# Kernel optimization log

Hardware: AMD Instinct MI355X
Metric: run time of the kernel (lower is better)

The kernel has to match this reference:

```python
import jax, jax.numpy as jnp
import numpy as np

EMBED_DIM = 1024
NUM_HEADS = 16
HEAD_DIM = EMBED_DIM // NUM_HEADS


def setup_inputs() -> dict:
    key = jax.random.key(0)
    ks = jax.random.split(key, 5)
    s = 0.02
    return {
        "x": jax.random.normal(ks[0], (2, 2048, EMBED_DIM), dtype=jnp.float32),
        "w_qkv": jax.random.normal(ks[1], (EMBED_DIM, 3 * EMBED_DIM), dtype=jnp.float32) * s,
        "b_qkv": jnp.zeros((3 * EMBED_DIM,), dtype=jnp.float32),
        "w_out": jax.random.normal(ks[2], (EMBED_DIM, EMBED_DIM), dtype=jnp.float32) * s,
        "b_out": jnp.zeros((EMBED_DIM,), dtype=jnp.float32),
    }


def reference(x, w_qkv, b_qkv, w_out, b_out):
    B, T, C = x.shape
    qkv = x @ w_qkv + b_qkv                       # [B,T,3C]
    q, k, v = jnp.split(qkv, 3, axis=-1)
    # [B,T,C] -> [B,H,T,Dh]
    def heads(t):
        return t.reshape(B, T, NUM_HEADS, HEAD_DIM).transpose(0, 2, 1, 3)
    q, k, v = heads(q), heads(k), heads(v)
    scale = 1.0 / np.sqrt(HEAD_DIM).astype(np.float32)
    scores = jnp.einsum("bhqd,bhkd->bhqk", q, k) * scale  # [B,H,T,T]
    causal = jnp.tril(jnp.ones((T, T), dtype=bool))
    scores = jnp.where(causal[None, None], scores, -jnp.inf)
    attn = jax.nn.softmax(scores, axis=-1)
    out = jnp.einsum("bhqk,bhkd->bhqd", attn, v)  # [B,H,T,Dh]
    out = out.transpose(0, 2, 1, 3).reshape(B, T, C)
    return out @ w_out + b_out
```

## Files before the change

kernel.cpp:

```cpp
#include <hip/hip_runtime.h>

typedef unsigned short u16;
typedef unsigned int u32;
typedef __attribute__((ext_vector_type(8))) short bf16x8;
typedef __attribute__((ext_vector_type(4))) float f32x4;

#define TOK   4096
#define EMB   1024
#define NQKV  3072
#define TSEQ  2048
#define NH    16

__device__ __forceinline__ u16 f2b(float f) {
  union { float f; unsigned u; } v; v.f = f;
  unsigned r = v.u + 0x7FFFu + ((v.u >> 16) & 1u);
  return (u16)(r >> 16);
}

__device__ __forceinline__ u32 pack_rn(float a, float b) {
  u32 ua = __float_as_uint(a) + 0x8000u;
  u32 ub = __float_as_uint(b) + 0x8000u;
  return __builtin_amdgcn_perm(ub, ua, 0x07060302u);
}


__global__ __launch_bounds__(256) void cvt_f32_bf16(const float* __restrict__ x,
                                                    u16* __restrict__ y, int n4) {
  int i = blockIdx.x * 256 + threadIdx.x;
  if (i < n4) {
    float4 v = ((const float4*)x)[i];
    union { u16 us[4]; uint2 u2; } o;
    o.us[0] = f2b(v.x); o.us[1] = f2b(v.y); o.us[2] = f2b(v.z); o.us[3] = f2b(v.w);
    ((uint2*)y)[i] = o.u2;
  }
}

__global__ __launch_bounds__(256) void transpose_f32_bf16(const float* __restrict__ src,
                                                          u16* __restrict__ dst,
                                                          int R, int C) {
  __shared__ u16 sm[64][65];
  int c0 = blockIdx.x * 64, r0 = blockIdx.y * 64;
  int tid = threadIdx.x;
#pragma unroll
  for (int i = 0; i < 16; i++) {
    int idx = tid + i * 256;
    int r = idx >> 6, c = idx & 63;
    sm[r][c] = f2b(src[(size_t)(r0 + r) * C + c0 + c]);
  }
  __syncthreads();
#pragma unroll
  for (int i = 0; i < 16; i++) {
    int idx = tid + i * 256;
    int cc = idx >> 6, rr = idx & 63;
    dst[(size_t)(c0 + cc) * R + r0 + rr] = sm[rr][cc];
  }
}

__global__ __launch_bounds__(256) void transpose_v(const u16* __restrict__ V,
                                                   u16* __restrict__ Vt) {
  __shared__ u16 sm[64][72];
  int t0 = blockIdx.x * 64, bh = blockIdx.y;
  size_t base = (size_t)bh * TSEQ * 64;
  int tid = threadIdx.x;
  int r = tid >> 2, c = (tid & 3) * 16;
  *(bf16x8*)&sm[r][c]     = *(const bf16x8*)&V[base + (size_t)(t0 + r) * 64 + c];
  *(bf16x8*)&sm[r][c + 8] = *(const bf16x8*)&V[base + (size_t)(t0 + r) * 64 + c + 8];
  __syncthreads();
  int d = tid >> 2, tc = (tid & 3) * 16;
  union { u16 us[16]; uint4 v4[2]; } o;
#pragma unroll
  for (int i = 0; i < 16; i++) o.us[i] = sm[tc + i][d];
  *(uint4*)&Vt[base + (size_t)d * TSEQ + t0 + tc]     = o.v4[0];
  *(uint4*)&Vt[base + (size_t)d * TSEQ + t0 + tc + 8] = o.v4[1];
}


template <int MODE, int TM>
__global__ __launch_bounds__(256) void gemm_bt(const u16* __restrict__ A,
                                               const u16* __restrict__ Bt,
                                               const float* __restrict__ bias,
                                               u16* __restrict__ qb, u16* __restrict__ kb,
                                               u16* __restrict__ vb, float* __restrict__ outp,
                                               int K, int N) {
  constexpr int LDA = 68;
  constexpr int CT = (TM == 128) ? 4 : 2;
  constexpr int AC = TM / 32;
  __shared__ u16 As[TM][LDA];
  __shared__ u16 Bs[128][LDA];
  int tid = threadIdx.x;
  int m0 = blockIdx.y * TM, n0 = blockIdx.x * 128;
  int lane = tid & 63, wid = tid >> 6;
  int wm = (TM == 128) ? (wid >> 1) * 64 : 0;
  int wn = (TM == 128) ? (wid & 1) * 64 : wid * 32;
  int l15 = lane & 15, quad = lane >> 4;
  int lrow = lane >> 3, lcol = (lane & 7) * 8;

  f32x4 acc[4][CT];
#pragma unroll
  for (int i = 0; i < 4; i++)
#pragma unroll
    for (int j = 0; j < CT; j++) acc[i][j] = (f32x4){0.f, 0.f, 0.f, 0.f};

  bf16x8 ar[AC], br[4];
#pragma unroll
  for (int i = 0; i < AC; i++)
    ar[i] = *(const bf16x8*)&A[(size_t)(m0 + (wid * AC + i) * 8 + lrow) * K + lcol];
#pragma unroll
  for (int i = 0; i < 4; i++)
    br[i] = *(const bf16x8*)&Bt[(size_t)(n0 + (wid * 4 + i) * 8 + lrow) * K + lcol];

  for (int k0 = 0; k0 < K; k0 += 64) {
#pragma unroll
    for (int i = 0; i < AC; i++)
      *(bf16x8*)&As[(wid * AC + i) * 8 + lrow][lcol] = ar[i];
#pragma unroll
    for (int i = 0; i < 4; i++)
      *(bf16x8*)&Bs[(wid * 4 + i) * 8 + lrow][lcol] = br[i];
    __syncthreads();

    if (k0 + 64 < K) {
      int kn = k0 + 64;
#pragma unroll
      for (int i = 0; i < AC; i++)
        ar[i] = *(const bf16x8*)&A[(size_t)(m0 + (wid * AC + i) * 8 + lrow) * K + kn + lcol];
#pragma unroll
      for (int i = 0; i < 4; i++)
        br[i] = *(const bf16x8*)&Bt[(size_t)(n0 + (wid * 4 + i) * 8 + lrow) * K + kn + lcol];
    }

#pragma unroll
    for (int ks = 0; ks < 2; ks++) {
      bf16x8 af[4], bfr[CT];
#pragma unroll
      for (int rt = 0; rt < 4; rt++)
        af[rt] = *(const bf16x8*)&As[wm + rt * 16 + l15][ks * 32 + quad * 8];
#pragma unroll
      for (int ct = 0; ct < CT; ct++)
        bfr[ct] = *(const bf16x8*)&Bs[wn + ct * 16 + l15][ks * 32 + quad * 8];
#pragma unroll
      for (int rt = 0; rt < 4; rt++)
#pragma unroll
        for (int ct = 0; ct < CT; ct++)
          acc[rt][ct] = __builtin_amdgcn_mfma_f32_16x16x32_bf16(bfr[ct], af[rt], acc[rt][ct], 0, 0, 0);
    }
    __syncthreads();
  }

#pragma unroll
  for (int rt = 0; rt < 4; rt++) {
#pragma unroll
    for (int ct = 0; ct < CT; ct++) {
      int m = m0 + wm + rt * 16 + l15;
      int nb = n0 + wn + ct * 16 + quad * 4;
      float4 b4 = *(const float4*)&bias[nb];
      float v0 = acc[rt][ct][0] + b4.x, v1 = acc[rt][ct][1] + b4.y;
      float v2 = acc[rt][ct][2] + b4.z, v3 = acc[rt][ct][3] + b4.w;
      if (MODE == 0) {
        int sel = nb >> 10;
        int c = nb & 1023;
        int h = c >> 6, d0 = c & 63;
        int b = m >> 11, t = m & 2047;
        u16* dst = (sel == 0) ? qb : (sel == 1) ? kb : vb;
        union { u32 u[2]; uint2 u2; } o;
        o.u[0] = pack_rn(v0, v1);
        o.u[1] = pack_rn(v2, v3);
        *(uint2*)&dst[((((size_t)b * NH + h) * TSEQ + t) << 6) + d0] = o.u2;
      } else {
        float4 o = {v0, v1, v2, v3};
        *(float4*)&outp[(size_t)m * N + nb] = o;
      }
    }
  }
}


__global__ __launch_bounds__(256) void attn_kernel(const u16* __restrict__ Qb,
                                                   const u16* __restrict__ Kb,
                                                   const u16* __restrict__ Vtb,
                                                   u16* __restrict__ O) {
  __shared__ u16 Ks[64][68];
  __shared__ u16 Vt[64][68];
  __shared__ u16 Ps[4][16][68];

  const float SCL = 0.18033688f;
  const float MOFF = 16.0f;

  int id = blockIdx.x;
  int bh = (id >> 5) & 31;
  int q5 = id & 31;
  int qt = ((id >> 8) & 1) ? (31 - q5) : q5;

  int tid = threadIdx.x, lane = tid & 63, w = tid >> 6;
  int l15 = lane & 15, quad = lane >> 4;
  const size_t hoff = (size_t)bh * TSEQ * 64;

  int qrow = qt * 64 + w * 16 + l15;
  bf16x8 qf[2];
  qf[0] = *(const bf16x8*)&Qb[hoff + (size_t)qrow * 64 + quad * 8];
  qf[1] = *(const bf16x8*)&Qb[hoff + (size_t)qrow * 64 + 32 + quad * 8];

  f32x4 acc[4];
#pragma unroll
  for (int i = 0; i < 4; i++) acc[i] = (f32x4){0.f, 0.f, 0.f, 0.f};
  float l_i = 0.f;

  int srow = tid >> 2, scol = (tid & 3) * 16;

  bf16x8 kr0, kr1, vr0, vr1;
  {
    size_t kg = hoff + (size_t)srow * 64;
    kr0 = *(const bf16x8*)&Kb[kg + scol];
    kr1 = *(const bf16x8*)&Kb[kg + scol + 8];
    size_t vg = hoff + (size_t)srow * TSEQ;
    vr0 = *(const bf16x8*)&Vtb[vg + scol];
    vr1 = *(const bf16x8*)&Vtb[vg + scol + 8];
  }

  for (int kt = 0; kt <= qt; kt++) {
    __syncthreads();
    *(bf16x8*)&Ks[srow][scol]     = kr0;
    *(bf16x8*)&Ks[srow][scol + 8] = kr1;
    *(bf16x8*)&Vt[srow][scol]     = vr0;
    *(bf16x8*)&Vt[srow][scol + 8] = vr1;
    __syncthreads();
    if (kt < qt) {
      size_t kg = hoff + (size_t)((kt + 1) * 64 + srow) * 64;
      kr0 = *(const bf16x8*)&Kb[kg + scol];
      kr1 = *(const bf16x8*)&Kb[kg + scol + 8];
      size_t vg = hoff + (size_t)srow * TSEQ + (kt + 1) * 64;
      vr0 = *(const bf16x8*)&Vtb[vg + scol];
      vr1 = *(const bf16x8*)&Vtb[vg + scol + 8];
    }

    f32x4 s[4];
#pragma unroll
    for (int ct = 0; ct < 4; ct++) s[ct] = (f32x4){0.f, 0.f, 0.f, 0.f};
#pragma unroll
    for (int ks = 0; ks < 2; ks++)
#pragma unroll
      for (int ct = 0; ct < 4; ct++) {
        bf16x8 kf = *(const bf16x8*)&Ks[ct * 16 + l15][ks * 32 + quad * 8];
        s[ct] = __builtin_amdgcn_mfma_f32_16x16x32_bf16(kf, qf[ks], s[ct], 0, 0, 0);
      }

    if (kt == qt) {
      int ql = w * 16 + l15;
#pragma unroll
      for (int ct = 0; ct < 4; ct++)
#pragma unroll
        for (int r = 0; r < 4; r++)
          if (ct * 16 + quad * 4 + r > ql) s[ct][r] = -1e30f;
    }

    float rs = 0.f;
#pragma unroll
    for (int ct = 0; ct < 4; ct++)
#pragma unroll
      for (int r = 0; r < 4; r++) {
        float p = exp2f(__builtin_fmaf(s[ct][r], SCL, -MOFF));
        s[ct][r] = p;
        rs += p;
      }
    l_i += rs;

#pragma unroll
    for (int ct = 0; ct < 4; ct++) {
      *(u32*)&Ps[w][l15][ct * 16 + quad * 4]     = pack_rn(s[ct][0], s[ct][1]);
      *(u32*)&Ps[w][l15][ct * 16 + quad * 4 + 2] = pack_rn(s[ct][2], s[ct][3]);
    }
    bf16x8 pf0 = *(const bf16x8*)&Ps[w][l15][quad * 8];
    bf16x8 pf1 = *(const bf16x8*)&Ps[w][l15][32 + quad * 8];
#pragma unroll
    for (int dt = 0; dt < 4; dt++) {
      bf16x8 vf0 = *(const bf16x8*)&Vt[dt * 16 + l15][quad * 8];
      bf16x8 vf1 = *(const bf16x8*)&Vt[dt * 16 + l15][32 + quad * 8];
      acc[dt] = __builtin_amdgcn_mfma_f32_16x16x32_bf16(vf0, pf0, acc[dt], 0, 0, 0);
      acc[dt] = __builtin_amdgcn_mfma_f32_16x16x32_bf16(vf1, pf1, acc[dt], 0, 0, 0);
    }
  }

  l_i += __shfl_xor(l_i, 16);
  l_i += __shfl_xor(l_i, 32);
  float inv = 1.0f / l_i;

  int b = bh >> 4, h = bh & 15;
  int qg = qt * 64 + w * 16 + l15;
  size_t rowbase = ((size_t)b * TSEQ + qg) * 1024 + h * 64;
#pragma unroll
  for (int dt = 0; dt < 4; dt++) {
    union { u32 u[2]; uint2 u2; } o;
    o.u[0] = pack_rn(acc[dt][0] * inv, acc[dt][1] * inv);
    o.u[1] = pack_rn(acc[dt][2] * inv, acc[dt][3] * inv);
    *(uint2*)&O[rowbase + dt * 16 + quad * 4] = o.u2;
  }
}


extern "C" void kernel_launch(void* const* d_in, const int* in_sizes, int n_in,
                              void* d_out, int out_size, void* d_ws, size_t ws_size,
                              hipStream_t stream) {
  (void)in_sizes; (void)n_in; (void)out_size; (void)ws_size;
  const float* x     = (const float*)d_in[0];
  const float* w_qkv = (const float*)d_in[1];
  const float* b_qkv = (const float*)d_in[2];
  const float* w_out = (const float*)d_in[3];
  const float* b_out = (const float*)d_in[4];
  float* out = (float*)d_out;

  char* p = (char*)d_ws;
  u16* x_bf  = (u16*)p; p += (size_t)TOK * EMB * 2;
  u16* wqkvT = (u16*)p; p += (size_t)NQKV * EMB * 2;
  u16* woutT = (u16*)p; p += (size_t)EMB * EMB * 2;
  u16* Qb    = (u16*)p; p += (size_t)32 * TSEQ * 64 * 2;
  u16* Kb    = (u16*)p; p += (size_t)32 * TSEQ * 64 * 2;
  u16* Vraw  = (u16*)p; p += (size_t)32 * TSEQ * 64 * 2;
  u16* attn_o = (u16*)p;
  u16* Vtb   = x_bf;

  cvt_f32_bf16<<<dim3(TOK * EMB / 1024), 256, 0, stream>>>(x, x_bf, TOK * EMB / 4);
  transpose_f32_bf16<<<dim3(NQKV / 64, EMB / 64), 256, 0, stream>>>(w_qkv, wqkvT, EMB, NQKV);
  transpose_f32_bf16<<<dim3(EMB / 64, EMB / 64), 256, 0, stream>>>(w_out, woutT, EMB, EMB);
  gemm_bt<0, 128><<<dim3(NQKV / 128, TOK / 128), 256, 0, stream>>>(x_bf, wqkvT, b_qkv,
                                                                   Qb, Kb, Vraw, nullptr, EMB, NQKV);
  transpose_v<<<dim3(TSEQ / 64, 32), 256, 0, stream>>>(Vraw, Vtb);
  attn_kernel<<<dim3(1024), 256, 0, stream>>>(Qb, Kb, Vtb, attn_o);
  gemm_bt<1, 64><<<dim3(EMB / 128, TOK / 64), 256, 0, stream>>>(attn_o, woutT, b_out,
                                                                nullptr, nullptr, nullptr, out, EMB, EMB);
}
```

Before: 195.3 us.

## Load K/V fragments directly from global in attention and fuse prep kernels

The attention kernel no longer stages K and V tiles through shared memory with block-wide barriers. Each wave now reads its MFMA operand fragments straight from global memory, relying on L1/L2 to serve the reuse across the four waves. The P stores to shared memory are widened to 64-bit writes. Separately, the input conversion and the two weight transposes are merged into one launch to cut launch overhead. The trade-off is fewer syncs and less LDS traffic against redundant, less coalesced global loads and no explicit prefetch of the next tile.

```diff
diff --git a/kernel.cpp b/kernel.cpp
--- a/kernel.cpp
+++ b/kernel.cpp
@@ -24,23 +24,31 @@
 }
 
 
-__global__ __launch_bounds__(256) void cvt_f32_bf16(const float* __restrict__ x,
-                                                    u16* __restrict__ y, int n4) {
-  int i = blockIdx.x * 256 + threadIdx.x;
-  if (i < n4) {
+__global__ __launch_bounds__(256) void prep_kernel(const float* __restrict__ x,
+                                                   u16* __restrict__ x_bf,
+                                                   const float* __restrict__ w_qkv,
+                                                   u16* __restrict__ wqkvT,
+                                                   const float* __restrict__ w_out,
+                                                   u16* __restrict__ woutT) {
+  __shared__ u16 sm[64][65];
+  int bid = blockIdx.x, tid = threadIdx.x;
+  if (bid < 4096) {
+    int i = bid * 256 + tid;
     float4 v = ((const float4*)x)[i];
     union { u16 us[4]; uint2 u2; } o;
     o.us[0] = f2b(v.x); o.us[1] = f2b(v.y); o.us[2] = f2b(v.z); o.us[3] = f2b(v.w);
-    ((uint2*)y)[i] = o.u2;
-  }
-}
-
-__global__ __launch_bounds__(256) void transpose_f32_bf16(const float* __restrict__ src,
-                                                          u16* __restrict__ dst,
-                                                          int R, int C) {
-  __shared__ u16 sm[64][65];
-  int c0 = blockIdx.x * 64, r0 = blockIdx.y * 64;
-  int tid = threadIdx.x;
+    ((uint2*)x_bf)[i] = o.u2;
+    return;
+  }
+  const float* src; u16* dst; int R, C, bx, by;
+  if (bid < 4096 + 768) {
+    int t = bid - 4096; bx = t % 48; by = t / 48;
+    src = w_qkv; dst = wqkvT; R = EMB; C = NQKV;
+  } else {
+    int t = bid - 4096 - 768; bx = t & 15; by = t >> 4;
+    src = w_out; dst = woutT; R = EMB; C = EMB;
+  }
+  int c0 = bx * 64, r0 = by * 64;
 #pragma unroll
   for (int i = 0; i < 16; i++) {
     int idx = tid + i * 256;
@@ -178,8 +186,6 @@
                                                    const u16* __restrict__ Kb,
                                                    const u16* __restrict__ Vtb,
                                                    u16* __restrict__ O) {
-  __shared__ u16 Ks[64][68];
-  __shared__ u16 Vt[64][68];
   __shared__ u16 Ps[4][16][68];
 
   const float SCL = 0.18033688f;
@@ -204,44 +210,19 @@
   for (int i = 0; i < 4; i++) acc[i] = (f32x4){0.f, 0.f, 0.f, 0.f};
   float l_i = 0.f;
 
-  int srow = tid >> 2, scol = (tid & 3) * 16;
-
-  bf16x8 kr0, kr1, vr0, vr1;
-  {
-    size_t kg = hoff + (size_t)srow * 64;
-    kr0 = *(const bf16x8*)&Kb[kg + scol];
-    kr1 = *(const bf16x8*)&Kb[kg + scol + 8];
-    size_t vg = hoff + (size_t)srow * TSEQ;
-    vr0 = *(const bf16x8*)&Vtb[vg + scol];
-    vr1 = *(const bf16x8*)&Vtb[vg + scol + 8];
-  }
+  const u16* kp = Kb + hoff + (size_t)l15 * 64 + quad * 8;
+  const u16* vp = Vtb + hoff + (size_t)l15 * TSEQ + quad * 8;
 
   for (int kt = 0; kt <= qt; kt++) {
-    __syncthreads();
-    *(bf16x8*)&Ks[srow][scol]     = kr0;
-    *(bf16x8*)&Ks[srow][scol + 8] = kr1;
-    *(bf16x8*)&Vt[srow][scol]     = vr0;
-    *(bf16x8*)&Vt[srow][scol + 8] = vr1;
-    __syncthreads();
-    if (kt < qt) {
-      size_t kg = hoff + (size_t)((kt + 1) * 64 + srow) * 64;
-      kr0 = *(const bf16x8*)&Kb[kg + scol];
-      kr1 = *(const bf16x8*)&Kb[kg + scol + 8];
-      size_t vg = hoff + (size_t)srow * TSEQ + (kt + 1) * 64;
-      vr0 = *(const bf16x8*)&Vtb[vg + scol];
-      vr1 = *(const bf16x8*)&Vtb[vg + scol + 8];
-    }
-
     f32x4 s[4];
 #pragma unroll
-    for (int ct = 0; ct < 4; ct++) s[ct] = (f32x4){0.f, 0.f, 0.f, 0.f};
-#pragma unroll
-    for (int ks = 0; ks < 2; ks++)
-#pragma unroll
-      for (int ct = 0; ct < 4; ct++) {
-        bf16x8 kf = *(const bf16x8*)&Ks[ct * 16 + l15][ks * 32 + quad * 8];
-        s[ct] = __builtin_amdgcn_mfma_f32_16x16x32_bf16(kf, qf[ks], s[ct], 0, 0, 0);
-      }
+    for (int ct = 0; ct < 4; ct++) {
+      bf16x8 kf0 = *(const bf16x8*)&kp[ct * 16 * 64];
+      bf16x8 kf1 = *(const bf16x8*)&kp[ct * 16 * 64 + 32];
+      f32x4 z = (f32x4){0.f, 0.f, 0.f, 0.f};
+      z = __builtin_amdgcn_mfma_f32_16x16x32_bf16(kf0, qf[0], z, 0, 0, 0);
+      s[ct] = __builtin_amdgcn_mfma_f32_16x16x32_bf16(kf1, qf[1], z, 0, 0, 0);
+    }
 
     if (kt == qt) {
       int ql = w * 16 + l15;
@@ -265,18 +246,23 @@
 
 #pragma unroll
     for (int ct = 0; ct < 4; ct++) {
-      *(u32*)&Ps[w][l15][ct * 16 + quad * 4]     = pack_rn(s[ct][0], s[ct][1]);
-      *(u32*)&Ps[w][l15][ct * 16 + quad * 4 + 2] = pack_rn(s[ct][2], s[ct][3]);
+      union { u32 u[2]; uint2 u2; } o;
+      o.u[0] = pack_rn(s[ct][0], s[ct][1]);
+      o.u[1] = pack_rn(s[ct][2], s[ct][3]);
+      *(uint2*)&Ps[w][l15][ct * 16 + quad * 4] = o.u2;
     }
     bf16x8 pf0 = *(const bf16x8*)&Ps[w][l15][quad * 8];
     bf16x8 pf1 = *(const bf16x8*)&Ps[w][l15][32 + quad * 8];
 #pragma unroll
     for (int dt = 0; dt < 4; dt++) {
-      bf16x8 vf0 = *(const bf16x8*)&Vt[dt * 16 + l15][quad * 8];
-      bf16x8 vf1 = *(const bf16x8*)&Vt[dt * 16 + l15][32 + quad * 8];
+      bf16x8 vf0 = *(const bf16x8*)&vp[(size_t)dt * 16 * TSEQ];
+      bf16x8 vf1 = *(const bf16x8*)&vp[(size_t)dt * 16 * TSEQ + 32];
       acc[dt] = __builtin_amdgcn_mfma_f32_16x16x32_bf16(vf0, pf0, acc[dt], 0, 0, 0);
       acc[dt] = __builtin_amdgcn_mfma_f32_16x16x32_bf16(vf1, pf1, acc[dt], 0, 0, 0);
     }
+
+    kp += 64 * 64;
+    vp += 64;
   }
 
   l_i += __shfl_xor(l_i, 16);
@@ -317,9 +303,7 @@
   u16* attn_o = (u16*)p;
   u16* Vtb   = x_bf;
 
-  cvt_f32_bf16<<<dim3(TOK * EMB / 1024), 256, 0, stream>>>(x, x_bf, TOK * EMB / 4);
-  transpose_f32_bf16<<<dim3(NQKV / 64, EMB / 64), 256, 0, stream>>>(w_qkv, wqkvT, EMB, NQKV);
-  transpose_f32_bf16<<<dim3(EMB / 64, EMB / 64), 256, 0, stream>>>(w_out, woutT, EMB, EMB);
+  prep_kernel<<<dim3(4096 + 768 + 256), 256, 0, stream>>>(x, x_bf, w_qkv, wqkvT, w_out, woutT);
   gemm_bt<0, 128><<<dim3(NQKV / 128, TOK / 128), 256, 0, stream>>>(x_bf, wqkvT, b_qkv,
                                                                    Qb, Kb, Vraw, nullptr, EMB, NQKV);
   transpose_v<<<dim3(TSEQ / 64, 32), 256, 0, stream>>>(Vraw, Vtb);
```

New measurement: 269.3 us. +37.9%, slower.

## Double query tile per attention block and merge prep kernels into one launch

Applied to the files above, without the earlier changes.

The attention kernel now handles 128 query rows per block, with each wave owning two 16-row query groups, so every K/V tile staged in shared memory serves twice as many queries. The grid is halved to 512 blocks and remapped so paired query tiles balance the causal work. The three input conversion and transpose kernels are merged into one launch to save launch overhead. The cost is more registers per wave and fewer blocks, which may reduce occupancy and latency hiding.

```diff
diff --git a/kernel.cpp b/kernel.cpp
--- a/kernel.cpp
+++ b/kernel.cpp
@@ -24,23 +24,31 @@
 }
 
 
-__global__ __launch_bounds__(256) void cvt_f32_bf16(const float* __restrict__ x,
-                                                    u16* __restrict__ y, int n4) {
-  int i = blockIdx.x * 256 + threadIdx.x;
-  if (i < n4) {
+__global__ __launch_bounds__(256) void prep_kernel(const float* __restrict__ x,
+                                                   u16* __restrict__ x_bf,
+                                                   const float* __restrict__ w_qkv,
+                                                   u16* __restrict__ wqkvT,
+                                                   const float* __restrict__ w_out,
+                                                   u16* __restrict__ woutT) {
+  __shared__ u16 sm[64][65];
+  int bid = blockIdx.x, tid = threadIdx.x;
+  if (bid < 4096) {
+    int i = bid * 256 + tid;
     float4 v = ((const float4*)x)[i];
     union { u16 us[4]; uint2 u2; } o;
     o.us[0] = f2b(v.x); o.us[1] = f2b(v.y); o.us[2] = f2b(v.z); o.us[3] = f2b(v.w);
-    ((uint2*)y)[i] = o.u2;
-  }
-}
-
-__global__ __launch_bounds__(256) void transpose_f32_bf16(const float* __restrict__ src,
-                                                          u16* __restrict__ dst,
-                                                          int R, int C) {
-  __shared__ u16 sm[64][65];
-  int c0 = blockIdx.x * 64, r0 = blockIdx.y * 64;
-  int tid = threadIdx.x;
+    ((uint2*)x_bf)[i] = o.u2;
+    return;
+  }
+  const float* src; u16* dst; int R, C, bx, by;
+  if (bid < 4096 + 768) {
+    int t = bid - 4096; bx = t % 48; by = t / 48;
+    src = w_qkv; dst = wqkvT; R = EMB; C = NQKV;
+  } else {
+    int t = bid - 4096 - 768; bx = t & 15; by = t >> 4;
+    src = w_out; dst = woutT; R = EMB; C = EMB;
+  }
+  int c0 = bx * 64, r0 = by * 64;
 #pragma unroll
   for (int i = 0; i < 16; i++) {
     int idx = tid + i * 256;
@@ -180,31 +188,40 @@
                                                    u16* __restrict__ O) {
   __shared__ u16 Ks[64][68];
   __shared__ u16 Vt[64][68];
-  __shared__ u16 Ps[4][16][68];
+  __shared__ u16 Ps[4][2][16][68];
 
   const float SCL = 0.18033688f;
   const float MOFF = 16.0f;
 
   int id = blockIdx.x;
-  int bh = (id >> 5) & 31;
-  int q5 = id & 31;
-  int qt = ((id >> 8) & 1) ? (31 - q5) : q5;
+  int bh = id & 31;
+  int qq = id >> 5;
+  int Qt = (qq < 8) ? qq : 23 - qq;
 
   int tid = threadIdx.x, lane = tid & 63, w = tid >> 6;
   int l15 = lane & 15, quad = lane >> 4;
   const size_t hoff = (size_t)bh * TSEQ * 64;
 
-  int qrow = qt * 64 + w * 16 + l15;
-  bf16x8 qf[2];
-  qf[0] = *(const bf16x8*)&Qb[hoff + (size_t)qrow * 64 + quad * 8];
-  qf[1] = *(const bf16x8*)&Qb[hoff + (size_t)qrow * 64 + 32 + quad * 8];
-
-  f32x4 acc[4];
-#pragma unroll
-  for (int i = 0; i < 4; i++) acc[i] = (f32x4){0.f, 0.f, 0.f, 0.f};
-  float l_i = 0.f;
+  int q0 = Qt * 128 + w * 32;
+  bf16x8 qfA0, qfA1, qfB0, qfB1;
+  {
+    const u16* qp = Qb + hoff + (size_t)(q0 + l15) * 64 + quad * 8;
+    qfA0 = *(const bf16x8*)qp;
+    qfA1 = *(const bf16x8*)(qp + 32);
+    qfB0 = *(const bf16x8*)(qp + 16 * 64);
+    qfB1 = *(const bf16x8*)(qp + 16 * 64 + 32);
+  }
+
+  f32x4 accA[4], accB[4];
+#pragma unroll
+  for (int i = 0; i < 4; i++) {
+    accA[i] = (f32x4){0.f, 0.f, 0.f, 0.f};
+    accB[i] = (f32x4){0.f, 0.f, 0.f, 0.f};
+  }
+  float lA = 0.f, lB = 0.f;
 
   int srow = tid >> 2, scol = (tid & 3) * 16;
+  const int KT = 2 * Qt + 2;
 
   bf16x8 kr0, kr1, vr0, vr1;
   {
@@ -216,14 +233,14 @@
     vr1 = *(const bf16x8*)&Vtb[vg + scol + 8];
   }
 
-  for (int kt = 0; kt <= qt; kt++) {
+  for (int kt = 0; kt < KT; kt++) {
     __syncthreads();
     *(bf16x8*)&Ks[srow][scol]     = kr0;
     *(bf16x8*)&Ks[srow][scol + 8] = kr1;
     *(bf16x8*)&Vt[srow][scol]     = vr0;
     *(bf16x8*)&Vt[srow][scol + 8] = vr1;
     __syncthreads();
-    if (kt < qt) {
+    if (kt + 1 < KT) {
       size_t kg = hoff + (size_t)((kt + 1) * 64 + srow) * 64;
       kr0 = *(const bf16x8*)&Kb[kg + scol];
       kr1 = *(const bf16x8*)&Kb[kg + scol + 8];
@@ -232,66 +249,91 @@
       vr1 = *(const bf16x8*)&Vtb[vg + scol + 8];
     }
 
-    f32x4 s[4];
-#pragma unroll
-    for (int ct = 0; ct < 4; ct++) s[ct] = (f32x4){0.f, 0.f, 0.f, 0.f};
-#pragma unroll
-    for (int ks = 0; ks < 2; ks++)
-#pragma unroll
-      for (int ct = 0; ct < 4; ct++) {
-        bf16x8 kf = *(const bf16x8*)&Ks[ct * 16 + l15][ks * 32 + quad * 8];
-        s[ct] = __builtin_amdgcn_mfma_f32_16x16x32_bf16(kf, qf[ks], s[ct], 0, 0, 0);
+    f32x4 sA[4], sB[4];
+#pragma unroll
+    for (int ct = 0; ct < 4; ct++) {
+      bf16x8 kf0 = *(const bf16x8*)&Ks[ct * 16 + l15][quad * 8];
+      bf16x8 kf1 = *(const bf16x8*)&Ks[ct * 16 + l15][32 + quad * 8];
+      f32x4 z = (f32x4){0.f, 0.f, 0.f, 0.f};
+      z = __builtin_amdgcn_mfma_f32_16x16x32_bf16(kf0, qfA0, z, 0, 0, 0);
+      sA[ct] = __builtin_amdgcn_mfma_f32_16x16x32_bf16(kf1, qfA1, z, 0, 0, 0);
+      f32x4 y = (f32x4){0.f, 0.f, 0.f, 0.f};
+      y = __builtin_amdgcn_mfma_f32_16x16x32_bf16(kf0, qfB0, y, 0, 0, 0);
+      sB[ct] = __builtin_amdgcn_mfma_f32_16x16x32_bf16(kf1, qfB1, y, 0, 0, 0);
+    }
+
+    int kbase = kt * 64;
+    if (kbase + 63 > q0) {
+      int qg = q0 + l15;
+#pragma unroll
+      for (int ct = 0; ct < 4; ct++)
+#pragma unroll
+        for (int r = 0; r < 4; r++)
+          if (kbase + ct * 16 + quad * 4 + r > qg) sA[ct][r] = -1e30f;
+    }
+    if (kbase + 63 > q0 + 16) {
+      int qg = q0 + 16 + l15;
+#pragma unroll
+      for (int ct = 0; ct < 4; ct++)
+#pragma unroll
+        for (int r = 0; r < 4; r++)
+          if (kbase + ct * 16 + quad * 4 + r > qg) sB[ct][r] = -1e30f;
+    }
+
+    float rsA = 0.f, rsB = 0.f;
+#pragma unroll
+    for (int ct = 0; ct < 4; ct++)
+#pragma unroll
+      for (int r = 0; r < 4; r++) {
+        float pA = exp2f(__builtin_fmaf(sA[ct][r], SCL, -MOFF));
+        float pB = exp2f(__builtin_fmaf(sB[ct][r], SCL, -MOFF));
+        sA[ct][r] = pA; rsA += pA;
+        sB[ct][r] = pB; rsB += pB;
       }
-
-    if (kt == qt) {
-      int ql = w * 16 + l15;
-#pragma unroll
-      for (int ct = 0; ct < 4; ct++)
-#pragma unroll
-        for (int r = 0; r < 4; r++)
-          if (ct * 16 + quad * 4 + r > ql) s[ct][r] = -1e30f;
-    }
-
-    float rs = 0.f;
-#pragma unroll
-    for (int ct = 0; ct < 4; ct++)
-#pragma unroll
-      for (int r = 0; r < 4; r++) {
-        float p = exp2f(__builtin_fmaf(s[ct][r], SCL, -MOFF));
-        s[ct][r] = p;
-        rs += p;
-      }
-    l_i += rs;
+    lA += rsA; lB += rsB;
 
 #pragma unroll
     for (int ct = 0; ct < 4; ct++) {
-      *(u32*)&Ps[w][l15][ct * 16 + quad * 4]     = pack_rn(s[ct][0], s[ct][1]);
-      *(u32*)&Ps[w][l15][ct * 16 + quad * 4 + 2] = pack_rn(s[ct][2], s[ct][3]);
-    }
-    bf16x8 pf0 = *(const bf16x8*)&Ps[w][l15][quad * 8];
-    bf16x8 pf1 = *(const bf16x8*)&Ps[w][l15][32 + quad * 8];
+      union { u32 u[2]; uint2 u2; } oa, ob;
+      oa.u[0] = pack_rn(sA[ct][0], sA[ct][1]);
+      oa.u[1] = pack_rn(sA[ct][2], sA[ct][3]);
+      ob.u[0] = pack_rn(sB[ct][0], sB[ct][1]);
+      ob.u[1] = pack_rn(sB[ct][2], sB[ct][3]);
+      *(uint2*)&Ps[w][0][l15][ct * 16 + quad * 4] = oa.u2;
+      *(uint2*)&Ps[w][1][l15][ct * 16 + quad * 4] = ob.u2;
+    }
+    bf16x8 pfA0 = *(const bf16x8*)&Ps[w][0][l15][quad * 8];
+    bf16x8 pfA1 = *(const bf16x8*)&Ps[w][0][l15][32 + quad * 8];
+    bf16x8 pfB0 = *(const bf16x8*)&Ps[w][1][l15][quad * 8];
+    bf16x8 pfB1 = *(const bf16x8*)&Ps[w][1][l15][32 + quad * 8];
+
 #pragma unroll
     for (int dt = 0; dt < 4; dt++) {
       bf16x8 vf0 = *(const bf16x8*)&Vt[dt * 16 + l15][quad * 8];
       bf16x8 vf1 = *(const bf16x8*)&Vt[dt * 16 + l15][32 + quad * 8];
-      acc[dt] = __builtin_amdgcn_mfma_f32_16x16x32_bf16(vf0, pf0, acc[dt], 0, 0, 0);
-      acc[dt] = __builtin_amdgcn_mfma_f32_16x16x32_bf16(vf1, pf1, acc[dt], 0, 0, 0);
-    }
-  }
-
-  l_i += __shfl_xor(l_i, 16);
-  l_i += __shfl_xor(l_i, 32);
-  float inv = 1.0f / l_i;
+      accA[dt] = __builtin_amdgcn_mfma_f32_16x16x32_bf16(vf0, pfA0, accA[dt], 0, 0, 0);
+      accA[dt] = __builtin_amdgcn_mfma_f32_16x16x32_bf16(vf1, pfA1, accA[dt], 0, 0, 0);
+      accB[dt] = __builtin_amdgcn_mfma_f32_16x16x32_bf16(vf0, pfB0, accB[dt], 0, 0, 0);
+      accB[dt] = __builtin_amdgcn_mfma_f32_16x16x32_bf16(vf1, pfB1, accB[dt], 0, 0, 0);
+    }
+  }
+
+  lA += __shfl_xor(lA, 16); lA += __shfl_xor(lA, 32);
+  lB += __shfl_xor(lB, 16); lB += __shfl_xor(lB, 32);
+  float invA = 1.0f / lA, invB = 1.0f / lB;
 
   int b = bh >> 4, h = bh & 15;
-  int qg = qt * 64 + w * 16 + l15;
-  size_t rowbase = ((size_t)b * TSEQ + qg) * 1024 + h * 64;
+  size_t rowA = ((size_t)b * TSEQ + q0 + l15) * 1024 + h * 64;
+  size_t rowB = rowA + (size_t)16 * 1024;
 #pragma unroll
   for (int dt = 0; dt < 4; dt++) {
-    union { u32 u[2]; uint2 u2; } o;
-    o.u[0] = pack_rn(acc[dt][0] * inv, acc[dt][1] * inv);
-    o.u[1] = pack_rn(acc[dt][2] * inv, acc[dt][3] * inv);
-    *(uint2*)&O[rowbase + dt * 16 + quad * 4] = o.u2;
+    union { u32 u[2]; uint2 u2; } oa, ob;
+    oa.u[0] = pack_rn(accA[dt][0] * invA, accA[dt][1] * invA);
+    oa.u[1] = pack_rn(accA[dt][2] * invA, accA[dt][3] * invA);
+    ob.u[0] = pack_rn(accB[dt][0] * invB, accB[dt][1] * invB);
+    ob.u[1] = pack_rn(accB[dt][2] * invB, accB[dt][3] * invB);
+    *(uint2*)&O[rowA + dt * 16 + quad * 4] = oa.u2;
+    *(uint2*)&O[rowB + dt * 16 + quad * 4] = ob.u2;
   }
 }
 
@@ -317,13 +359,11 @@
   u16* attn_o = (u16*)p;
   u16* Vtb   = x_bf;
 
-  cvt_f32_bf16<<<dim3(TOK * EMB / 1024), 256, 0, stream>>>(x, x_bf, TOK * EMB / 4);
-  transpose_f32_bf16<<<dim3(NQKV / 64, EMB / 64), 256, 0, stream>>>(w_qkv, wqkvT, EMB, NQKV);
-  transpose_f32_bf16<<<dim3(EMB / 64, EMB / 64), 256, 0, stream>>>(w_out, woutT, EMB, EMB);
+  prep_kernel<<<dim3(4096 + 768 + 256), 256, 0, stream>>>(x, x_bf, w_qkv, wqkvT, w_out, woutT);
   gemm_bt<0, 128><<<dim3(NQKV / 128, TOK / 128), 256, 0, stream>>>(x_bf, wqkvT, b_qkv,
                                                                    Qb, Kb, Vraw, nullptr, EMB, NQKV);
   transpose_v<<<dim3(TSEQ / 64, 32), 256, 0, stream>>>(Vraw, Vtb);
-  attn_kernel<<<dim3(1024), 256, 0, stream>>>(Qb, Kb, Vtb, attn_o);
+  attn_kernel<<<dim3(512), 256, 0, stream>>>(Qb, Kb, Vtb, attn_o);
   gemm_bt<1, 64><<<dim3(EMB / 128, TOK / 64), 256, 0, stream>>>(attn_o, woutT, b_out,
                                                                 nullptr, nullptr, nullptr, out, EMB, EMB);
 }
```

Measured after the change: 200.6 us. 2.7% more time.
